# Optimization experiments

Measured on AMD Instinct MI355X. Metric: run time of the kernel, lower is better.

The kernel has to match this reference:

```python
import jax, jax.numpy as jnp
import numpy as np

N, IN_F, OUT_F, K = 256, 8192, 8320, 16
J = OUT_F - IN_F  # 128


def setup_inputs() -> dict:
    key = jax.random.key(0)
    k1, k2 = jax.random.split(key)
    tensor = jax.random.normal(k1, (N, IN_F), dtype=jnp.float32)
    T = jax.random.normal(k2, (IN_F, J, K), dtype=jnp.float32)
    return {"tensor": tensor, "T": T}


def reference(tensor, T):
    # flatten(start_dim=1) is identity for rank-2 input
    x = tensor.reshape(tensor.shape[0], -1)            # [N, IN_F]
    feats = jnp.einsum('ni,ijk->njk', x, T)            # [N, J, K]
    # pairwise L1 across batch: [N,1,J,K] - [N,J,K] -> [N,N,J,K]
    diff = jnp.abs(feats[:, None, :, :] - feats[None, :, :, :])
    l1 = jnp.sum(diff, axis=3)                         # [N, N, J]
    diversity = jnp.sum(jnp.exp(-l1), axis=1)          # [N, J]
    return jnp.concatenate((x, diversity), axis=1)     # [N, IN_F + J]
```

## Files before the change

### kernel.cpp

```cpp
#include <hip/hip_runtime.h>

typedef unsigned int  u32;
typedef unsigned short u16;

typedef __bf16 bf16x8 __attribute__((ext_vector_type(8)));
typedef float  floatx4 __attribute__((ext_vector_type(4)));

#define N_ROWS 256
#define IN_F   8192
#define OUT_F  8320
#define JDIM   128
#define KDIM   16
#define JK     2048

#define BM     128
#define BN     64
#define BK     64

typedef const __attribute__((address_space(1))) u32 gu32;
typedef __attribute__((address_space(3))) u32 su32;

__device__ __forceinline__ u16 f2bf(float f) {
    u32 u = __float_as_uint(f);
    return (u16)((u + 0x7fffu + ((u >> 16) & 1u)) >> 16);
}
__device__ __forceinline__ float bf2f(u16 h) { return __uint_as_float(((u32)h) << 16); }

__global__ __launch_bounds__(256) void prep_kernel(const float* __restrict__ X,
                                                   float* __restrict__ out,
                                                   u16* __restrict__ Xb)
{
    int t = blockIdx.x * 256 + threadIdx.x;
    float4 v = reinterpret_cast<const float4*>(X)[t];
    int row = t >> 11;
    int c4  = t & 2047;
    reinterpret_cast<float4*>(out + (size_t)row * OUT_F)[c4] = v;
    ushort4 b;
    b.x = f2bf(v.x); b.y = f2bf(v.y); b.z = f2bf(v.z); b.w = f2bf(v.w);
    reinterpret_cast<ushort4*>(Xb)[t] = b;
    if (t < 8192) {
        int r2 = t >> 5, j4 = t & 31;
        reinterpret_cast<float4*>(out + (size_t)r2 * OUT_F + IN_F)[j4] = make_float4(0.f, 0.f, 0.f, 0.f);
    }
}

__global__ __launch_bounds__(256, 4) void gemm_kernel(const u16* __restrict__ Xb,
                                                      const float* __restrict__ W,
                                                      u16* __restrict__ slabs,
                                                      int kchunk)
{
    __shared__ u16 xs[BM * BK];
    __shared__ u16 wt[BN * BK];

    const int tid  = threadIdx.x;
    const int lane = tid & 63;
    const int wave = tid >> 6;
    const int c0   = blockIdx.x * BN;
    const int row0 = blockIdx.y * BM;
    const int s    = blockIdx.z;
    const int k0base = s * kchunk;

    floatx4 acc[2][4] = {};

    const int xrl = lane >> 3;
    const int xgc = (lane & 7) ^ xrl;
    const int wcol = lane;
    const int wkh  = wave;

    const int iters = kchunk >> 6;
    for (int it = 0; it < iters; ++it) {
        const int k0 = k0base + it * BK;
        __syncthreads();

        #pragma unroll
        for (int g = 0; g < 4; ++g) {
            int rbase = wave * 32 + g * 8;
            const u16* gp = Xb + (size_t)(row0 + rbase + xrl) * IN_F + k0 + xgc * 8;
            u32* lp = (u32*)&xs[rbase * BK];
            __builtin_amdgcn_global_load_lds((gu32*)gp, (su32*)lp, 16, 0, 0);
        }

        u32 pk[2][4];
        #pragma unroll
        for (int cc = 0; cc < 2; ++cc) {
            int chunk = wkh * 2 + cc;
            const float* wp = W + (size_t)(k0 + chunk * 8) * JK + c0 + wcol;
            #pragma unroll
            for (int p = 0; p < 4; ++p) {
                float w0 = wp[(size_t)(2 * p) * JK];
                float w1 = wp[(size_t)(2 * p + 1) * JK];
                pk[cc][p] = (u32)f2bf(w0) | ((u32)f2bf(w1) << 16);
            }
        }
        #pragma unroll
        for (int cc = 0; cc < 2; ++cc) {
            int chunk = wkh * 2 + cc;
            int slot  = chunk ^ (wcol & 7);
            *(uint4*)&wt[wcol * BK + slot * 8] = *(uint4*)pk[cc];
        }
        __syncthreads();

        const int mrow = lane & 15;
        const int q    = lane >> 4;
        #pragma unroll
        for (int h = 0; h < 2; ++h) {
            bf16x8 a[2], b[4];
            #pragma unroll
            for (int rt = 0; rt < 2; ++rt) {
                int rl   = wave * 32 + rt * 16 + mrow;
                int slot = (h * 4 + q) ^ (rl & 7);
                a[rt] = *reinterpret_cast<const bf16x8*>(&xs[rl * BK + slot * 8]);
            }
            #pragma unroll
            for (int ct = 0; ct < 4; ++ct) {
                int col  = ct * 16 + mrow;
                int slot = (h * 4 + q) ^ (col & 7);
                b[ct] = *reinterpret_cast<const bf16x8*>(&wt[col * BK + slot * 8]);
            }
            #pragma unroll
            for (int rt = 0; rt < 2; ++rt)
                #pragma unroll
                for (int ct = 0; ct < 4; ++ct)
                    acc[rt][ct] = __builtin_amdgcn_mfma_f32_16x16x32_bf16(a[rt], b[ct], acc[rt][ct], 0, 0, 0);
        }
    }

    const int qe = lane >> 4;
    const int cl = lane & 15;
    u16* sp = slabs + (size_t)s * N_ROWS * JK;
    #pragma unroll
    for (int rt = 0; rt < 2; ++rt)
        #pragma unroll
        for (int ct = 0; ct < 4; ++ct)
            #pragma unroll
            for (int r = 0; r < 4; ++r) {
                int row = row0 + wave * 32 + rt * 16 + qe * 4 + r;
                int col = c0 + ct * 16 + cl;
                sp[(size_t)row * JK + col] = f2bf(acc[rt][ct][r]);
            }
}

__global__ __launch_bounds__(256) void reduce_kernel(const u16* __restrict__ slabs,
                                                     float* __restrict__ feats, int S)
{
    int t = blockIdx.x * 256 + threadIdx.x;
    float acc[8] = {};
    for (int s = 0; s < S; ++s) {
        uint4 v = *(const uint4*)(slabs + (size_t)s * N_ROWS * JK + (size_t)t * 8);
        const u16* h = (const u16*)&v;
        #pragma unroll
        for (int e = 0; e < 8; ++e) acc[e] += bf2f(h[e]);
    }
    float4* fp = (float4*)(feats + (size_t)t * 8);
    fp[0] = make_float4(acc[0], acc[1], acc[2], acc[3]);
    fp[1] = make_float4(acc[4], acc[5], acc[6], acc[7]);
}

__global__ __launch_bounds__(256) void pairwise_kernel(const float* __restrict__ feats,
                                                       float* __restrict__ out)
{
    const int j = blockIdx.x;
    const int mq = blockIdx.y;
    const int n = threadIdx.x;

    __shared__ float F[N_ROWS * KDIM];
    const float* fr = feats + (size_t)n * JK + j * KDIM;
    float4 v0 = ((const float4*)fr)[0];
    float4 v1 = ((const float4*)fr)[1];
    float4 v2 = ((const float4*)fr)[2];
    float4 v3 = ((const float4*)fr)[3];
    float4* Fp = (float4*)&F[n * KDIM];
    Fp[0] = v0; Fp[1] = v1; Fp[2] = v2; Fp[3] = v3;
    __syncthreads();

    float f[16] = { v0.x, v0.y, v0.z, v0.w, v1.x, v1.y, v1.z, v1.w,
                    v2.x, v2.y, v2.z, v2.w, v3.x, v3.y, v3.z, v3.w };
    float accum = 0.f;
    const int m0 = mq * 64;
    for (int m = 0; m < 64; ++m) {
        const float* Fm = &F[(m0 + m) * KDIM];
        float l1 = 0.f;
        #pragma unroll
        for (int k = 0; k < 16; ++k) l1 += fabsf(f[k] - Fm[k]);
        accum += exp2f(-1.4426950408889634f * l1);
    }
    atomicAdd(&out[(size_t)n * OUT_F + IN_F + j], accum);
}

extern "C" void kernel_launch(void* const* d_in, const int* in_sizes, int n_in,
                              void* d_out, int out_size, void* d_ws, size_t ws_size,
                              hipStream_t stream)
{
    const float* X = (const float*)d_in[0];
    const float* T = (const float*)d_in[1];
    float* out = (float*)d_out;

    float* feats = (float*)d_ws;
    u16*   Xb    = (u16*)((char*)d_ws + (2u << 20));
    u16*   slabs = (u16*)((char*)d_ws + (6u << 20));

    int S = 16;
    if (ws_size < (6u << 20) + (size_t)16 * N_ROWS * JK * 2) S = 8;
    if (ws_size < (6u << 20) + (size_t)8  * N_ROWS * JK * 2) S = 4;
    int kchunk = IN_F / S;

    prep_kernel<<<2048, 256, 0, stream>>>(X, out, Xb);
    gemm_kernel<<<dim3(JK / BN, N_ROWS / BM, S), 256, 0, stream>>>(Xb, T, slabs, kchunk);
    reduce_kernel<<<256, 256, 0, stream>>>(slabs, feats, S);
    pairwise_kernel<<<dim3(JDIM, 4), 256, 0, stream>>>(feats, out);
}
```

Baseline: 148.4 us.

## Cover all rows per GEMM block and register-prefetch W with float4 loads

The GEMM block now spans all 256 rows (BM=256), so each fp32 W element is read and converted once instead of twice. The grid drops its row dimension, which halves the block count. W is loaded as coalesced float4 into registers and the next tile is prefetched during the MFMA phase. The W LDS tile uses a padded stride of 72 in place of the XOR swizzle. Each thread holds a 4x4 accumulator tile, which raises register pressure and lowers occupancy (launch bounds no longer request 4 blocks), and with fewer blocks the GPU may be underfilled.

```diff
diff --git a/kernel.cpp b/kernel.cpp
--- a/kernel.cpp
+++ b/kernel.cpp
@@ -13,9 +13,10 @@
 #define KDIM   16
 #define JK     2048
 
-#define BM     128
+#define BM     256
 #define BN     64
 #define BK     64
+#define WSTRIDE 72
 
 typedef const __attribute__((address_space(1))) u32 gu32;
 typedef __attribute__((address_space(3))) u32 su32;
@@ -44,28 +45,34 @@
     }
 }
 
-__global__ __launch_bounds__(256, 4) void gemm_kernel(const u16* __restrict__ Xb,
-                                                      const float* __restrict__ W,
-                                                      u16* __restrict__ slabs,
-                                                      int kchunk)
+__global__ __launch_bounds__(256) void gemm_kernel(const u16* __restrict__ Xb,
+                                                   const float* __restrict__ W,
+                                                   u16* __restrict__ slabs,
+                                                   int kchunk)
 {
     __shared__ u16 xs[BM * BK];
-    __shared__ u16 wt[BN * BK];
+    __shared__ u16 wt[BN * WSTRIDE];
 
     const int tid  = threadIdx.x;
     const int lane = tid & 63;
     const int wave = tid >> 6;
     const int c0   = blockIdx.x * BN;
-    const int row0 = blockIdx.y * BM;
-    const int s    = blockIdx.z;
+    const int s    = blockIdx.y;
     const int k0base = s * kchunk;
 
-    floatx4 acc[2][4] = {};
+    floatx4 acc[4][4] = {};
 
     const int xrl = lane >> 3;
     const int xgc = (lane & 7) ^ xrl;
-    const int wcol = lane;
-    const int wkh  = wave;
+    const int wk  = (tid >> 4) << 2;
+    const int wc  = (tid & 15) << 2;
+
+    const float* wptr = W + (size_t)(k0base + wk) * JK + c0 + wc;
+
+    float4 wreg[4];
+    #pragma unroll
+    for (int r = 0; r < 4; ++r)
+        wreg[r] = *(const float4*)(wptr + (size_t)r * JK);
 
     const int iters = kchunk >> 6;
     for (int it = 0; it < iters; ++it) {
@@ -73,52 +80,50 @@
         __syncthreads();
 
         #pragma unroll
-        for (int g = 0; g < 4; ++g) {
-            int rbase = wave * 32 + g * 8;
-            const u16* gp = Xb + (size_t)(row0 + rbase + xrl) * IN_F + k0 + xgc * 8;
+        for (int g = 0; g < 8; ++g) {
+            int rbase = wave * 64 + g * 8;
+            const u16* gp = Xb + (size_t)(rbase + xrl) * IN_F + k0 + xgc * 8;
             u32* lp = (u32*)&xs[rbase * BK];
             __builtin_amdgcn_global_load_lds((gu32*)gp, (su32*)lp, 16, 0, 0);
         }
 
-        u32 pk[2][4];
-        #pragma unroll
-        for (int cc = 0; cc < 2; ++cc) {
-            int chunk = wkh * 2 + cc;
-            const float* wp = W + (size_t)(k0 + chunk * 8) * JK + c0 + wcol;
-            #pragma unroll
-            for (int p = 0; p < 4; ++p) {
-                float w0 = wp[(size_t)(2 * p) * JK];
-                float w1 = wp[(size_t)(2 * p + 1) * JK];
-                pk[cc][p] = (u32)f2bf(w0) | ((u32)f2bf(w1) << 16);
-            }
-        }
-        #pragma unroll
-        for (int cc = 0; cc < 2; ++cc) {
-            int chunk = wkh * 2 + cc;
-            int slot  = chunk ^ (wcol & 7);
-            *(uint4*)&wt[wcol * BK + slot * 8] = *(uint4*)pk[cc];
+        {
+            const float* wr = (const float*)wreg;
+            #pragma unroll
+            for (int i = 0; i < 4; ++i) {
+                u32 lo = (u32)f2bf(wr[0 * 4 + i]) | ((u32)f2bf(wr[1 * 4 + i]) << 16);
+                u32 hi = (u32)f2bf(wr[2 * 4 + i]) | ((u32)f2bf(wr[3 * 4 + i]) << 16);
+                uint2 v; v.x = lo; v.y = hi;
+                *(uint2*)&wt[(wc + i) * WSTRIDE + wk] = v;
+            }
         }
         __syncthreads();
+
+        if (it + 1 < iters) {
+            const float* wn = wptr + (size_t)(it + 1) * BK * JK;
+            #pragma unroll
+            for (int r = 0; r < 4; ++r)
+                wreg[r] = *(const float4*)(wn + (size_t)r * JK);
+        }
 
         const int mrow = lane & 15;
         const int q    = lane >> 4;
         #pragma unroll
         for (int h = 0; h < 2; ++h) {
-            bf16x8 a[2], b[4];
-            #pragma unroll
-            for (int rt = 0; rt < 2; ++rt) {
-                int rl   = wave * 32 + rt * 16 + mrow;
+            bf16x8 a[4], b[4];
+            #pragma unroll
+            for (int rt = 0; rt < 4; ++rt) {
+                int rl   = wave * 64 + rt * 16 + mrow;
                 int slot = (h * 4 + q) ^ (rl & 7);
                 a[rt] = *reinterpret_cast<const bf16x8*>(&xs[rl * BK + slot * 8]);
             }
             #pragma unroll
             for (int ct = 0; ct < 4; ++ct) {
-                int col  = ct * 16 + mrow;
-                int slot = (h * 4 + q) ^ (col & 7);
-                b[ct] = *reinterpret_cast<const bf16x8*>(&wt[col * BK + slot * 8]);
-            }
-            #pragma unroll
-            for (int rt = 0; rt < 2; ++rt)
+                int col = ct * 16 + mrow;
+                b[ct] = *reinterpret_cast<const bf16x8*>(&wt[col * WSTRIDE + (h * 4 + q) * 8]);
+            }
+            #pragma unroll
+            for (int rt = 0; rt < 4; ++rt)
                 #pragma unroll
                 for (int ct = 0; ct < 4; ++ct)
                     acc[rt][ct] = __builtin_amdgcn_mfma_f32_16x16x32_bf16(a[rt], b[ct], acc[rt][ct], 0, 0, 0);
@@ -129,12 +134,12 @@
     const int cl = lane & 15;
     u16* sp = slabs + (size_t)s * N_ROWS * JK;
     #pragma unroll
-    for (int rt = 0; rt < 2; ++rt)
+    for (int rt = 0; rt < 4; ++rt)
         #pragma unroll
         for (int ct = 0; ct < 4; ++ct)
             #pragma unroll
             for (int r = 0; r < 4; ++r) {
-                int row = row0 + wave * 32 + rt * 16 + qe * 4 + r;
+                int row = wave * 64 + rt * 16 + qe * 4 + r;
                 int col = c0 + ct * 16 + cl;
                 sp[(size_t)row * JK + col] = f2bf(acc[rt][ct][r]);
             }
@@ -205,7 +210,7 @@
     int kchunk = IN_F / S;
 
     prep_kernel<<<2048, 256, 0, stream>>>(X, out, Xb);
-    gemm_kernel<<<dim3(JK / BN, N_ROWS / BM, S), 256, 0, stream>>>(Xb, T, slabs, kchunk);
+    gemm_kernel<<<dim3(JK / BN, S), 256, 0, stream>>>(Xb, T, slabs, kchunk);
     reduce_kernel<<<256, 256, 0, stream>>>(slabs, feats, S);
     pairwise_kernel<<<dim3(JDIM, 4), 256, 0, stream>>>(feats, out);
 }
```

After: 139.0 us. 1.07x faster.
